# Kernel optimization log

Hardware: AMD Instinct MI355X
Metric: run time of the kernel (lower is better)

The kernel has to match this reference:

```python
import jax, jax.numpy as jnp
import numpy as np

B, N = 8192, 64
EPS = 1e-3  # diagonal jitter to guarantee SPD


def setup_inputs() -> dict:
    key = jax.random.key(0)
    A = jax.random.normal(key, (B, N, N), dtype=jnp.float32)
    # SPD: X = A A^T / N + eps*I  (eigenvalues strictly positive)
    X = jnp.einsum('bij,bkj->bik', A, A) / N + EPS * jnp.eye(N, dtype=jnp.float32)
    return {"X": X}


def reference(X) -> jnp.ndarray:
    # torch.linalg.eigh -> jnp.linalg.eigh (batched symmetric eigendecomposition)
    eigvals, eigvecs = jnp.linalg.eigh(X)            # [B,N], [B,N,N]
    log_eigvals = jnp.log(eigvals)                   # [B,N]
    # eigvecs @ diag(log_eigvals) @ eigvecs^T, fused as scaled-column GEMM
    return jnp.einsum('bik,bk,bjk->bij', eigvecs, log_eigvals, eigvecs)
```

## Files before the change

### kernel.cpp

```cpp
#include <hip/hip_runtime.h>
#include <cmath>


#define NMAT_PER_BLOCK 4
#define MAXSWEEP 18
#define JTOL 1e-5f
#define XTOL 5e-5f
#define TSTRIDE 68

typedef float f32x2 __attribute__((ext_vector_type(2)));

__global__ __launch_bounds__(256, 2)
void logeig_kernel(const float* __restrict__ X, float* __restrict__ Out, int B)
{
    const int wave = threadIdx.x >> 6;
    const int lane = threadIdx.x & 63;
    long b = (long)blockIdx.x * NMAT_PER_BLOCK + wave;
    if (b >= B) b = B - 1;

    __shared__ float Tlds[NMAT_PER_BLOCK][64 * TSTRIDE];
    __shared__ float wlds[NMAT_PER_BLOCK][64];

    const float* Xb = X + b * 4096;
    float*       Ob = Out + b * 4096;
    float*       T  = Tlds[wave];
    float4*      myrow = reinterpret_cast<float4*>(T + lane * TSTRIDE);

    f32x2 fv[32];
#pragma unroll
    for (int i = 0; i < 16; ++i) {
        const float4 v = reinterpret_cast<const float4*>(Xb + lane * 64)[i];
        fv[2*i+0] = f32x2{v.x, v.y};
        fv[2*i+1] = f32x2{v.z, v.w};
        myrow[i] = v;
    }
    __builtin_amdgcn_wave_barrier();

    float app;
    {
        f32x2 a0 = {0.f,0.f}, a1 = {0.f,0.f}, a2 = {0.f,0.f}, a3 = {0.f,0.f};
#pragma unroll
        for (int i = 0; i < 32; i += 4) {
            a0 = __builtin_elementwise_fma(fv[i+0], fv[i+0], a0);
            a1 = __builtin_elementwise_fma(fv[i+1], fv[i+1], a1);
            a2 = __builtin_elementwise_fma(fv[i+2], fv[i+2], a2);
            a3 = __builtin_elementwise_fma(fv[i+3], fv[i+3], a3);
        }
        const f32x2 at = (a0 + a1) + (a2 + a3);
        app = at.x + at.y;
    }

    for (int sweep = 0; sweep < MAXSWEEP; ++sweep) {
        bool big = false;
        for (int r = 1; r < 64; ++r) {
            const int partner = lane ^ r;

            const float aqq = __int_as_float(
                __builtin_amdgcn_ds_bpermute(partner << 2, __float_as_int(app)));

            const float4* pc = reinterpret_cast<const float4*>(T + partner * TSTRIDE);
            f32x2 tv[32];
#pragma unroll
            for (int i = 0; i < 16; ++i) {
                const float4 v = pc[i];
                tv[2*i+0] = f32x2{v.x, v.y};
                tv[2*i+1] = f32x2{v.z, v.w};
            }
#pragma unroll
            for (int i = 0; i < 32; ++i)
                asm volatile("" : "+v"(tv[i]));

            float apq;
            {
                f32x2 a0 = {0.f,0.f}, a1 = {0.f,0.f}, a2 = {0.f,0.f}, a3 = {0.f,0.f};
#pragma unroll
                for (int i = 0; i < 32; i += 4) {
                    a0 = __builtin_elementwise_fma(fv[i+0], tv[i+0], a0);
                    a1 = __builtin_elementwise_fma(fv[i+1], tv[i+1], a1);
                    a2 = __builtin_elementwise_fma(fv[i+2], tv[i+2], a2);
                    a3 = __builtin_elementwise_fma(fv[i+3], tv[i+3], a3);
                }
                const f32x2 at = (a0 + a1) + (a2 + a3);
                apq = at.x + at.y;
            }

            const float thr = sqrtf(app * aqq);
            const bool rot = fabsf(apq) > JTOL * thr;
            big = big || (fabsf(apq) > XTOL * thr);

            if (__any(rot)) {
                const bool  isp = lane < partner;
                const float App = isp ? app : aqq;
                const float Aqq = isp ? aqq : app;
                const float tau = (Aqq - App) / (2.f * apq);
                const float t0  = copysignf(1.f, tau) / (fabsf(tau) + sqrtf(fmaf(tau, tau, 1.f)));
                const float c0  = rsqrtf(fmaf(t0, t0, 1.f));
                const float s0  = t0 * c0;
                const float tl  = rot ? (isp ? t0 : -t0) : 0.f;
                const float c   = rot ? c0 : 1.f;
                const float sl  = rot ? (isp ? s0 : -s0) : 0.f;

                const f32x2 c2  = {c, c};
                const f32x2 ns2 = {-sl, -sl};
#pragma unroll
                for (int i = 0; i < 32; ++i)
                    fv[i] = __builtin_elementwise_fma(ns2, tv[i], c2 * fv[i]);
                app = fmaf(-tl, apq, app);

                if (rot) {
#pragma unroll
                    for (int i = 0; i < 16; ++i)
                        myrow[i] = float4{fv[2*i+0].x, fv[2*i+0].y,
                                          fv[2*i+1].x, fv[2*i+1].y};
                }
            }
            __builtin_amdgcn_wave_barrier();
        }
        if (!__any(big)) break;
    }

    float nrm2;
    {
        f32x2 a0 = {0.f,0.f}, a1 = {0.f,0.f}, a2 = {0.f,0.f}, a3 = {0.f,0.f};
#pragma unroll
        for (int i = 0; i < 32; i += 4) {
            a0 = __builtin_elementwise_fma(fv[i+0], fv[i+0], a0);
            a1 = __builtin_elementwise_fma(fv[i+1], fv[i+1], a1);
            a2 = __builtin_elementwise_fma(fv[i+2], fv[i+2], a2);
            a3 = __builtin_elementwise_fma(fv[i+3], fv[i+3], a3);
        }
        const f32x2 at = (a0 + a1) + (a2 + a3);
        nrm2 = at.x + at.y;
    }
    const float wk  = 0.5f * logf(nrm2);
    const float inv = rsqrtf(nrm2);

#pragma unroll
    for (int i = 0; i < 16; ++i) {
        myrow[i] = float4{fv[2*i+0].x * inv, fv[2*i+0].y * inv,
                          fv[2*i+1].x * inv, fv[2*i+1].y * inv};
    }
    wlds[wave][lane] = wk;
    __syncthreads();

    const int la = lane >> 3, lb = lane & 7;
    float acc[8][8];
#pragma unroll
    for (int r0 = 0; r0 < 8; ++r0)
#pragma unroll
        for (int c0 = 0; c0 < 8; ++c0) acc[r0][c0] = 0.f;

    const float* wv = wlds[wave];
#pragma unroll 4
    for (int k = 0; k < 64; ++k) {
        const float wkk = wv[k];
        const float* row = T + k * TSTRIDE;
        const float4 p0 = *reinterpret_cast<const float4*>(row + la * 8);
        const float4 p1 = *reinterpret_cast<const float4*>(row + la * 8 + 4);
        const float4 u0 = *reinterpret_cast<const float4*>(row + lb * 8);
        const float4 u1 = *reinterpret_cast<const float4*>(row + lb * 8 + 4);
        const float pr[8] = { p0.x*wkk, p0.y*wkk, p0.z*wkk, p0.w*wkk,
                              p1.x*wkk, p1.y*wkk, p1.z*wkk, p1.w*wkk };
        const float uc[8] = { u0.x, u0.y, u0.z, u0.w, u1.x, u1.y, u1.z, u1.w };
#pragma unroll
        for (int r0 = 0; r0 < 8; ++r0)
#pragma unroll
            for (int c0 = 0; c0 < 8; ++c0)
                acc[r0][c0] = fmaf(pr[r0], uc[c0], acc[r0][c0]);
    }

#pragma unroll
    for (int r0 = 0; r0 < 8; ++r0) {
        float* dst = Ob + (la * 8 + r0) * 64 + lb * 8;
        float4 o0 = { acc[r0][0], acc[r0][1], acc[r0][2], acc[r0][3] };
        float4 o1 = { acc[r0][4], acc[r0][5], acc[r0][6], acc[r0][7] };
        reinterpret_cast<float4*>(dst)[0] = o0;
        reinterpret_cast<float4*>(dst)[1] = o1;
    }
}

extern "C" void kernel_launch(void* const* d_in, const int* in_sizes, int n_in,
                              void* d_out, int out_size, void* d_ws, size_t ws_size,
                              hipStream_t stream)
{
    const float* Xp = (const float*)d_in[0];
    float* Op = (float*)d_out;
    const int B = in_sizes[0] / 4096;
    const int grid = (B + NMAT_PER_BLOCK - 1) / NMAT_PER_BLOCK;
    logeig_kernel<<<grid, 256, 0, stream>>>(Xp, Op, B);
}
```

Before: 3.202 ms.

## Use fast-scaled (square-root-free) Jacobi rotations, one matrix per wave block

```diff
diff --git a/kernel.cpp b/kernel.cpp
--- a/kernel.cpp
+++ b/kernel.cpp
@@ -2,28 +2,24 @@
 #include <cmath>
 
 
-#define NMAT_PER_BLOCK 4
-#define MAXSWEEP 18
-#define JTOL 1e-5f
-#define XTOL 5e-5f
+#define MAXSWEEP 16
+#define JTOL 1e-4f
+#define XTOL 5e-4f
 #define TSTRIDE 68
 
 typedef float f32x2 __attribute__((ext_vector_type(2)));
 
-__global__ __launch_bounds__(256, 2)
+__global__ __launch_bounds__(64, 4)
 void logeig_kernel(const float* __restrict__ X, float* __restrict__ Out, int B)
 {
-    const int wave = threadIdx.x >> 6;
     const int lane = threadIdx.x & 63;
-    long b = (long)blockIdx.x * NMAT_PER_BLOCK + wave;
-    if (b >= B) b = B - 1;
+    const long b = blockIdx.x;
 
-    __shared__ float Tlds[NMAT_PER_BLOCK][64 * TSTRIDE];
-    __shared__ float wlds[NMAT_PER_BLOCK][64];
+    __shared__ float T[64 * TSTRIDE];
+    __shared__ float wlds[64];
 
     const float* Xb = X + b * 4096;
     float*       Ob = Out + b * 4096;
-    float*       T  = Tlds[wave];
     float4*      myrow = reinterpret_cast<float4*>(T + lane * TSTRIDE);
 
     f32x2 fv[32];
@@ -49,14 +45,18 @@
         const f32x2 at = (a0 + a1) + (a2 + a3);
         app = at.x + at.y;
     }
+    float rho = 1.0f;
 
     for (int sweep = 0; sweep < MAXSWEEP; ++sweep) {
         bool big = false;
         for (int r = 1; r < 64; ++r) {
             const int partner = lane ^ r;
+            const int pa = partner << 2;
 
-            const float aqq = __int_as_float(
-                __builtin_amdgcn_ds_bpermute(partner << 2, __float_as_int(app)));
+            const float aqq  = __int_as_float(
+                __builtin_amdgcn_ds_bpermute(pa, __float_as_int(app)));
+            const float rhoq = __int_as_float(
+                __builtin_amdgcn_ds_bpermute(pa, __float_as_int(rho)));
 
             const float4* pc = reinterpret_cast<const float4*>(T + partner * TSTRIDE);
             f32x2 tv[32];
@@ -84,28 +84,30 @@
                 apq = at.x + at.y;
             }
 
-            const float thr = sqrtf(app * aqq);
-            const bool rot = fabsf(apq) > JTOL * thr;
-            big = big || (fabsf(apq) > XTOL * thr);
+            const float rel = sqrtf(app * aqq);
+            const bool rot = fabsf(apq) > JTOL * rel;
+            big = big || (fabsf(apq) > XTOL * rel);
 
             if (__any(rot)) {
-                const bool  isp = lane < partner;
-                const float App = isp ? app : aqq;
-                const float Aqq = isp ? aqq : app;
-                const float tau = (Aqq - App) / (2.f * apq);
+                const bool  isp  = lane < partner;
+                const float tapp = (rho  * rho ) * app;
+                const float taqq = (rhoq * rhoq) * aqq;
+                const float prod = (rho * rhoq) * apq;
+                const float App = isp ? tapp : taqq;
+                const float Aqq = isp ? taqq : tapp;
+                const float tau = (Aqq - App) / (2.f * prod);
                 const float t0  = copysignf(1.f, tau) / (fabsf(tau) + sqrtf(fmaf(tau, tau, 1.f)));
                 const float c0  = rsqrtf(fmaf(t0, t0, 1.f));
-                const float s0  = t0 * c0;
-                const float tl  = rot ? (isp ? t0 : -t0) : 0.f;
-                const float c   = rot ? c0 : 1.f;
-                const float sl  = rot ? (isp ? s0 : -s0) : 0.f;
+                const float tl  = isp ? t0 : -t0;
+                const float alpha = rot ? tl * (rhoq * __builtin_amdgcn_rcpf(rho)) : 0.f;
 
-                const f32x2 c2  = {c, c};
-                const f32x2 ns2 = {-sl, -sl};
+                const f32x2 na2 = {-alpha, -alpha};
 #pragma unroll
                 for (int i = 0; i < 32; ++i)
-                    fv[i] = __builtin_elementwise_fma(ns2, tv[i], c2 * fv[i]);
-                app = fmaf(-tl, apq, app);
+                    fv[i] = __builtin_elementwise_fma(na2, tv[i], fv[i]);
+
+                app = rot ? (app - alpha * apq) * fmaf(t0, t0, 1.f) : app;
+                rho = rot ? rho * c0 : rho;
 
                 if (rot) {
 #pragma unroll
@@ -132,15 +134,14 @@
         const f32x2 at = (a0 + a1) + (a2 + a3);
         nrm2 = at.x + at.y;
     }
-    const float wk  = 0.5f * logf(nrm2);
+    const float wk  = 0.5f * logf((rho * rho) * nrm2);
     const float inv = rsqrtf(nrm2);
 
 #pragma unroll
-    for (int i = 0; i < 16; ++i) {
+    for (int i = 0; i < 16; ++i)
         myrow[i] = float4{fv[2*i+0].x * inv, fv[2*i+0].y * inv,
                           fv[2*i+1].x * inv, fv[2*i+1].y * inv};
-    }
-    wlds[wave][lane] = wk;
+    wlds[lane] = wk;
     __syncthreads();
 
     const int la = lane >> 3, lb = lane & 7;
@@ -150,10 +151,9 @@
 #pragma unroll
         for (int c0 = 0; c0 < 8; ++c0) acc[r0][c0] = 0.f;
 
-    const float* wv = wlds[wave];
 #pragma unroll 4
     for (int k = 0; k < 64; ++k) {
-        const float wkk = wv[k];
+        const float wkk = wlds[k];
         const float* row = T + k * TSTRIDE;
         const float4 p0 = *reinterpret_cast<const float4*>(row + la * 8);
         const float4 p1 = *reinterpret_cast<const float4*>(row + la * 8 + 4);
@@ -186,6 +186,5 @@
     const float* Xp = (const float*)d_in[0];
     float* Op = (float*)d_out;
     const int B = in_sizes[0] / 4096;
-    const int grid = (B + NMAT_PER_BLOCK - 1) / NMAT_PER_BLOCK;
-    logeig_kernel<<<grid, 256, 0, stream>>>(Xp, Op, B);
+    logeig_kernel<<<B, 64, 0, stream>>>(Xp, Op, B);
 }
```

Result: no change. 3.141 ms (-1.9%).
